# Optimization experiments

Hardware: AMD Instinct MI355X
Metric: run time of the kernel (lower is better)

The kernel has to match this reference:

```python
import jax, jax.numpy as jnp
import numpy as np

B, H, W, C, NUM_HEADS = 32, 8, 128, 512, 8
HK, WK = 7, 11  # local_k
N = H * W
HEAD_DIM = C // NUM_HEADS
SCALE = HEAD_DIM ** (-0.5)


def make_local_mask():
    # key (i,j) is visible to query (h,w) iff i+HK//2 in [h, h+HK) and j+WK//2 in [w, w+WK)
    dh = jnp.arange(H)[None, :] - jnp.arange(H)[:, None] + HK // 2  # [H(query), H(key)]
    dw = jnp.arange(W)[None, :] - jnp.arange(W)[:, None] + WK // 2  # [W(query), W(key)]
    ok_h = (dh >= 0) & (dh < HK)
    ok_w = (dw >= 0) & (dw < WK)
    ok = ok_h[:, None, :, None] & ok_w[None, :, None, :]  # [H,W,H,W]
    return jnp.where(ok.reshape(N, N), 0.0, -jnp.inf).astype(jnp.float32)


def setup_inputs() -> dict:
    key = jax.random.key(0)
    k1, k2, k3 = jax.random.split(key, 3)
    s = C ** (-0.5)
    return {
        "x": jax.random.normal(k1, (B, N, C), dtype=jnp.float32),
        "w_qkv": jax.random.normal(k2, (C, 3 * C), dtype=jnp.float32) * s,
        "w_proj": jax.random.normal(k3, (C, C), dtype=jnp.float32) * s,
        "b_proj": jnp.zeros((C,), dtype=jnp.float32),
    }


def reference(x, w_qkv, w_proj, b_proj):
    mask = make_local_mask()  # [N, N], 0 in window, -inf outside
    b, n, c = x.shape
    qkv = (x @ w_qkv).reshape(b, n, 3, NUM_HEADS, HEAD_DIM)
    qkv = jnp.transpose(qkv, (2, 0, 3, 1, 4))  # [3, B, heads, N, head_dim]
    q, k, v = qkv[0], qkv[1], qkv[2]
    attn = jnp.einsum('bhqd,bhkd->bhqk', q, k) * SCALE + mask
    attn = jax.nn.softmax(attn, axis=-1)
    out = jnp.einsum('bhqk,bhkd->bhqd', attn, v)
    out = jnp.transpose(out, (0, 2, 1, 3)).reshape(b, n, c)
    return out @ w_proj + b_proj
```

## Files before the change

### kernel.cpp

```cpp
#include <hip/hip_runtime.h>

#define Bsz   32
#define Hh    8
#define Ww    128
#define Cc    512
#define NHEAD 8
#define HD    64
#define NN    1024
#define SCALE 0.125f
#define ROWS  1536

typedef _Float16 f16x8 __attribute__((ext_vector_type(8)));
typedef float    f32x4 __attribute__((ext_vector_type(4)));

__device__ __forceinline__ void gload16(const _Float16* g, _Float16* l) {
#if __has_builtin(__builtin_amdgcn_global_load_lds)
  __builtin_amdgcn_global_load_lds(
      (const __attribute__((address_space(1))) unsigned int*)g,
      (__attribute__((address_space(3))) unsigned int*)l, 16, 0, 0);
#else
  *(uint4*)l = *(const uint4*)g;
#endif
}

__global__ __launch_bounds__(256) void tcvt(
    const float* __restrict__ in, _Float16* __restrict__ out, int Nn, int K) {
  const int id = blockIdx.x * 256 + threadIdx.x;
  if (id < Nn * K) {
    const int n = id / K, k = id - n * K;
    out[id] = (_Float16)in[(size_t)k * Nn + n];
  }
}

template<bool A_F32, bool OUT_F16, bool HAS_BIAS>
__global__ __launch_bounds__(256, 2) void gemm_mfma(
    const void* __restrict__ Ap,
    const _Float16* __restrict__ BT,
    const float* __restrict__ bias,
    void* __restrict__ Cout,
    int nbx, int Nn, int K)
{
  __shared__ _Float16 As[2][128 * 32];
  __shared__ _Float16 Bs[2][128 * 32];

  const int wg    = blockIdx.x;
  const int chunk = gridDim.x >> 3;
  const int nid   = (wg & 7) * chunk + (wg >> 3);
  const int bn    = (nid % nbx) * 128;
  const int bm    = (nid / nbx) * 128;

  const int t  = threadIdx.x;
  const int l  = t & 63, wv = t >> 6;
  const int wr = wv >> 1, wc = wv & 1;

  f32x4 acc[4][4] = {};

  const int arow = t >> 2;
  const int ac   = (t & 3) * 8;

  float4 a0, a1, a2, a3;

  const float*    Af = (const float*)Ap;
  const _Float16* Ah = (const _Float16*)Ap;

  auto issueA = [&](int k0) {
    const float* s0 = &Af[(size_t)(bm + arow)      * K + k0 + ac];
    const float* s1 = &Af[(size_t)(bm + arow + 64) * K + k0 + ac];
    a0 = *(const float4*)s0; a1 = *(const float4*)(s0 + 4);
    a2 = *(const float4*)s1; a3 = *(const float4*)(s1 + 4);
  };
  auto writeA = [&](int pb) {
    union { _Float16 h[8]; uint4 u; } p0, p1;
    p0.h[0] = (_Float16)a0.x; p0.h[1] = (_Float16)a0.y;
    p0.h[2] = (_Float16)a0.z; p0.h[3] = (_Float16)a0.w;
    p0.h[4] = (_Float16)a1.x; p0.h[5] = (_Float16)a1.y;
    p0.h[6] = (_Float16)a1.z; p0.h[7] = (_Float16)a1.w;
    p1.h[0] = (_Float16)a2.x; p1.h[1] = (_Float16)a2.y;
    p1.h[2] = (_Float16)a2.z; p1.h[3] = (_Float16)a2.w;
    p1.h[4] = (_Float16)a3.x; p1.h[5] = (_Float16)a3.y;
    p1.h[6] = (_Float16)a3.z; p1.h[7] = (_Float16)a3.w;
    *(uint4*)&As[pb][arow * 32 + ac]        = p0.u;
    *(uint4*)&As[pb][(arow + 64) * 32 + ac] = p1.u;
  };
  auto gloadA = [&](int k0, int pb) {
    gload16(Ah + (size_t)(bm + arow)      * K + k0 + ac, &As[pb][t * 8]);
    gload16(Ah + (size_t)(bm + 64 + arow) * K + k0 + ac, &As[pb][2048 + t * 8]);
  };
  auto gloadB = [&](int k0, int pb) {
    gload16(BT + (size_t)(bn + arow)      * K + k0 + ac, &Bs[pb][t * 8]);
    gload16(BT + (size_t)(bn + 64 + arow) * K + k0 + ac, &Bs[pb][2048 + t * 8]);
  };

  const int nt = K / 32;

  if constexpr (A_F32) { issueA(0); writeA(0); }
  else                 { gloadA(0, 0); }
  gloadB(0, 0);
  __syncthreads();

  int buf = 0;
  for (int tt = 0; tt < nt; ++tt) {
    const int k0n = (tt + 1) * 32;
    const bool more = (tt + 1 < nt);
    if (more) {
      if constexpr (A_F32) issueA(k0n);
      else                 gloadA(k0n, buf ^ 1);
      gloadB(k0n, buf ^ 1);
    }

    const int rA = l & 15, ks = (l >> 4) * 8;
    f16x8 aF[4], bF[4];
#pragma unroll
    for (int i = 0; i < 4; ++i)
      aF[i] = *(const f16x8*)&As[buf][(wr * 64 + i * 16 + rA) * 32 + ks];
#pragma unroll
    for (int j = 0; j < 4; ++j)
      bF[j] = *(const f16x8*)&Bs[buf][(wc * 64 + j * 16 + rA) * 32 + ks];
#pragma unroll
    for (int i = 0; i < 4; ++i)
#pragma unroll
      for (int j = 0; j < 4; ++j)
        acc[i][j] = __builtin_amdgcn_mfma_f32_16x16x32_f16(aF[i], bF[j], acc[i][j], 0, 0, 0);

    if (more) {
      if constexpr (A_F32) writeA(buf ^ 1);
    }
    __syncthreads();
    buf ^= 1;
  }

  const int lc = l & 15, lr4 = (l >> 4) * 4;
#pragma unroll
  for (int i = 0; i < 4; ++i) {
    const size_t row0 = (size_t)(bm + wr * 64 + i * 16 + lr4);
#pragma unroll
    for (int j = 0; j < 4; ++j) {
      const int col = bn + wc * 64 + j * 16 + lc;
      const float bv = HAS_BIAS ? bias[col] : 0.f;
#pragma unroll
      for (int r = 0; r < 4; ++r) {
        const float v = acc[i][j][r] + bv;
        if (OUT_F16)
          ((_Float16*)Cout)[(row0 + r) * Nn + col] = (_Float16)v;
        else
          ((float*)Cout)[(row0 + r) * Nn + col] = v;
      }
    }
  }
}

__global__ __launch_bounds__(512, 4) void local_attn_mfma(
    const _Float16* __restrict__ qkv, _Float16* __restrict__ outh)
{
  const int wg  = blockIdx.x + (Hh / 2) * (blockIdx.y + NHEAD * blockIdx.z);
  const int nid = ((wg & 7) << 7) + (wg >> 3);
  const int hp = nid & 3, head = (nid >> 2) & 7, b = nid >> 5;
  const int h0 = hp * 2;

  const int t = threadIdx.x;
  const int wv = t >> 6, l = t & 63;
  const int g = l >> 4, c = l & 15;
  const int w0 = wv * 16;
  const int kb = min(max(w0 - 8, 0), 96);

  __shared__ _Float16 Vsh[64 * 132];
  __shared__ _Float16 Pbuf[8][576];

  const _Float16* qb = qkv + (size_t)b * NN * ROWS;

  f16x8 qF[2][2];
#pragma unroll
  for (int hi = 0; hi < 2; ++hi) {
    const _Float16* Qg = qb + (size_t)((h0 + hi) * Ww + w0 + c) * ROWS + head * HD;
    qF[hi][0] = *(const f16x8*)&Qg[g * 8];
    qF[hi][1] = *(const f16x8*)&Qg[32 + g * 8];
  }

  float mbias[2][4];
#pragma unroll
  for (int tt = 0; tt < 2; ++tt)
#pragma unroll
    for (int r = 0; r < 4; ++r) {
      const int kcol = kb + 16 * tt + 4 * g + r;
      const int qq   = w0 + c;
      mbias[tt][r] = (kcol >= qq - 5 && kcol <= qq + 5) ? 0.f : -1e30f;
    }

  const int r0 = max(0, h0 - 3), r1 = min(Hh - 1, h0 + 4);
  float m_run[2] = {-1e30f, -1e30f}, s_run[2] = {0.f, 0.f};
  f32x4 accO[2][4] = {};

  const int dd = t & 7, cg = (t & 255) >> 3;

  for (int kr = r0; kr <= r1; ++kr) {
    __syncthreads();
    if (t < 256) {
      f16x8 vr[4];
      const _Float16* Vg = qb + (size_t)(kr * Ww + cg * 4) * ROWS + 2 * Cc + head * HD + dd * 8;
#pragma unroll
      for (int i = 0; i < 4; ++i)
        vr[i] = *(const f16x8*)&Vg[(size_t)i * ROWS];
#pragma unroll
      for (int e = 0; e < 8; ++e) {
        union { _Float16 hh[4]; uint2 u; } pk;
        pk.hh[0] = vr[0][e]; pk.hh[1] = vr[1][e];
        pk.hh[2] = vr[2][e]; pk.hh[3] = vr[3][e];
        *(uint2*)&Vsh[(dd * 8 + e) * 132 + cg * 4] = pk.u;
      }
    }
    __syncthreads();

    const _Float16* Kg = qb + (size_t)(kr * Ww) * ROWS + Cc + head * HD;

#pragma unroll
    for (int hi = 0; hi < 2; ++hi) {
      const int hq = h0 + hi;
      if (kr < hq - 3 || kr > hq + 3) continue;

      f32x4 accS[2] = {};
#pragma unroll
      for (int tt = 0; tt < 2; ++tt) {
        const int col = kb + 16 * tt + c;
#pragma unroll
        for (int s = 0; s < 2; ++s) {
          const f16x8 kF = *(const f16x8*)&Kg[(size_t)col * ROWS + (s * 4 + g) * 8];
          accS[tt] = __builtin_amdgcn_mfma_f32_16x16x32_f16(kF, qF[hi][s], accS[tt], 0, 0, 0);
        }
      }

      float sc[2][4];
      float smax = -1e30f;
#pragma unroll
      for (int tt = 0; tt < 2; ++tt)
#pragma unroll
        for (int r = 0; r < 4; ++r) {
          sc[tt][r] = __builtin_fmaf(accS[tt][r], SCALE, mbias[tt][r]);
          smax = fmaxf(smax, sc[tt][r]);
        }
      smax = fmaxf(smax, __shfl_xor(smax, 16));
      smax = fmaxf(smax, __shfl_xor(smax, 32));
      const float mnew  = fmaxf(m_run[hi], smax);
      const float alpha = __expf(m_run[hi] - mnew);
      m_run[hi] = mnew;

      float ps = 0.f;
#pragma unroll
      for (int tt = 0; tt < 2; ++tt) {
        float p0 = __expf(sc[tt][0] - mnew), p1 = __expf(sc[tt][1] - mnew);
        float p2 = __expf(sc[tt][2] - mnew), p3 = __expf(sc[tt][3] - mnew);
        ps += (p0 + p1) + (p2 + p3);
        union { _Float16 hh[4]; uint2 u; } pk;
        pk.hh[0] = (_Float16)p0; pk.hh[1] = (_Float16)p1;
        pk.hh[2] = (_Float16)p2; pk.hh[3] = (_Float16)p3;
        *(uint2*)&Pbuf[wv][c * 36 + 16 * tt + 4 * g] = pk.u;
      }
      ps += __shfl_xor(ps, 16);
      ps += __shfl_xor(ps, 32);
      s_run[hi] = s_run[hi] * alpha + ps;

      float alr[4];
#pragma unroll
      for (int r = 0; r < 4; ++r)
        alr[r] = __shfl(alpha, 4 * g + r, 16);

      asm volatile("s_waitcnt lgkmcnt(0)" ::: "memory");

      union { f16x8 v; uint2 u2[2]; } pF;
      {
        const _Float16* pp = &Pbuf[wv][c * 36 + g * 8];
        pF.u2[0] = *(const uint2*)pp;
        pF.u2[1] = *(const uint2*)(pp + 4);
      }
#pragma unroll
      for (int jj = 0; jj < 4; ++jj)
#pragma unroll
        for (int r = 0; r < 4; ++r) accO[hi][jj][r] *= alr[r];
#pragma unroll
      for (int jj = 0; jj < 4; ++jj) {
        union { f16x8 v; uint2 u2[2]; } vF;
        const _Float16* vp = &Vsh[(16 * jj + c) * 132 + kb + g * 8];
        vF.u2[0] = *(const uint2*)vp;
        vF.u2[1] = *(const uint2*)(vp + 4);
        accO[hi][jj] = __builtin_amdgcn_mfma_f32_16x16x32_f16(pF.v, vF.v, accO[hi][jj], 0, 0, 0);
      }
    }
  }

#pragma unroll
  for (int hi = 0; hi < 2; ++hi) {
    _Float16* ob = outh + ((size_t)b * NN + (h0 + hi) * Ww + w0) * Cc + head * HD;
#pragma unroll
    for (int r = 0; r < 4; ++r) {
      const float sr  = __shfl(s_run[hi], 4 * g + r, 16);
      const float inv = 1.f / sr;
      const int q = 4 * g + r;
#pragma unroll
      for (int jj = 0; jj < 4; ++jj)
        ob[(size_t)q * Cc + 16 * jj + c] = (_Float16)(accO[hi][jj][r] * inv);
    }
  }
}

extern "C" void kernel_launch(void* const* d_in, const int* in_sizes, int n_in,
                              void* d_out, int out_size, void* d_ws, size_t ws_size,
                              hipStream_t stream)
{
  const float* x      = (const float*)d_in[0];
  const float* w_qkv  = (const float*)d_in[1];
  const float* w_proj = (const float*)d_in[2];
  const float* b_proj = (const float*)d_in[3];
  float* out = (float*)d_out;

  const int M = Bsz * NN;
  char* ws = (char*)d_ws;
  _Float16* qkvh  = (_Float16*)ws;
  _Float16* attnh = (_Float16*)(ws + 100663296);
  _Float16* wqT   = (_Float16*)(ws + 134217728);
  _Float16* wpT   = (_Float16*)(ws + 134217728 + 1572864);

  tcvt<<<(ROWS * Cc + 255) / 256, 256, 0, stream>>>(w_qkv, wqT, ROWS, Cc);
  tcvt<<<(Cc * Cc + 255) / 256, 256, 0, stream>>>(w_proj, wpT, Cc, Cc);

  gemm_mfma<true, true, false><<<(ROWS / 128) * (M / 128), 256, 0, stream>>>(
      x, wqT, nullptr, qkvh, ROWS / 128, ROWS, Cc);

  local_attn_mfma<<<dim3(Hh / 2, NHEAD, Bsz), 512, 0, stream>>>(qkvh, attnh);

  gemm_mfma<false, false, true><<<(Cc / 128) * (M / 128), 256, 0, stream>>>(
      attnh, wpT, b_proj, out, Cc / 128, Cc, Cc);
}
```

Measured before the change: 194.4 us.

## Widen GEMM tiles to 128x256 with 512 threads and prefetch V rows in attention

The two projection GEMMs now use 512-thread blocks covering 128x256 output tiles with eight waves in a 2x4 layout, halving block count and sharing each A tile across more columns. The local attention kernel prefetches the next key row's V into registers while computing the current row, then writes it to shared memory between explicit barriers instead of loading it synchronously at the top of each iteration. It also raises wave priority around the MFMA sections. The risks are higher register pressure from the occupancy-4 launch bound and fewer blocks in flight for the small projection GEMM.

```diff
diff --git a/kernel.cpp b/kernel.cpp
--- a/kernel.cpp
+++ b/kernel.cpp
@@ -33,7 +33,7 @@
 }
 
 template<bool A_F32, bool OUT_F16, bool HAS_BIAS>
-__global__ __launch_bounds__(256, 2) void gemm_mfma(
+__global__ __launch_bounds__(512, 4) void gemm_mfma(
     const void* __restrict__ Ap,
     const _Float16* __restrict__ BT,
     const float* __restrict__ bias,
@@ -41,54 +41,45 @@
     int nbx, int Nn, int K)
 {
   __shared__ _Float16 As[2][128 * 32];
-  __shared__ _Float16 Bs[2][128 * 32];
+  __shared__ _Float16 Bs[2][256 * 32];
 
   const int wg    = blockIdx.x;
   const int chunk = gridDim.x >> 3;
   const int nid   = (wg & 7) * chunk + (wg >> 3);
-  const int bn    = (nid % nbx) * 128;
+  const int bn    = (nid % nbx) * 256;
   const int bm    = (nid / nbx) * 128;
 
   const int t  = threadIdx.x;
   const int l  = t & 63, wv = t >> 6;
-  const int wr = wv >> 1, wc = wv & 1;
+  const int wr = wv >> 2, wc = wv & 3;
 
   f32x4 acc[4][4] = {};
 
   const int arow = t >> 2;
   const int ac   = (t & 3) * 8;
 
-  float4 a0, a1, a2, a3;
-
   const float*    Af = (const float*)Ap;
   const _Float16* Ah = (const _Float16*)Ap;
 
+  float4 a0, a1;
   auto issueA = [&](int k0) {
-    const float* s0 = &Af[(size_t)(bm + arow)      * K + k0 + ac];
-    const float* s1 = &Af[(size_t)(bm + arow + 64) * K + k0 + ac];
+    const float* s0 = &Af[(size_t)(bm + arow) * K + k0 + ac];
     a0 = *(const float4*)s0; a1 = *(const float4*)(s0 + 4);
-    a2 = *(const float4*)s1; a3 = *(const float4*)(s1 + 4);
   };
   auto writeA = [&](int pb) {
-    union { _Float16 h[8]; uint4 u; } p0, p1;
-    p0.h[0] = (_Float16)a0.x; p0.h[1] = (_Float16)a0.y;
-    p0.h[2] = (_Float16)a0.z; p0.h[3] = (_Float16)a0.w;
-    p0.h[4] = (_Float16)a1.x; p0.h[5] = (_Float16)a1.y;
-    p0.h[6] = (_Float16)a1.z; p0.h[7] = (_Float16)a1.w;
-    p1.h[0] = (_Float16)a2.x; p1.h[1] = (_Float16)a2.y;
-    p1.h[2] = (_Float16)a2.z; p1.h[3] = (_Float16)a2.w;
-    p1.h[4] = (_Float16)a3.x; p1.h[5] = (_Float16)a3.y;
-    p1.h[6] = (_Float16)a3.z; p1.h[7] = (_Float16)a3.w;
-    *(uint4*)&As[pb][arow * 32 + ac]        = p0.u;
-    *(uint4*)&As[pb][(arow + 64) * 32 + ac] = p1.u;
+    union { _Float16 h[8]; uint4 u; } pk;
+    pk.h[0] = (_Float16)a0.x; pk.h[1] = (_Float16)a0.y;
+    pk.h[2] = (_Float16)a0.z; pk.h[3] = (_Float16)a0.w;
+    pk.h[4] = (_Float16)a1.x; pk.h[5] = (_Float16)a1.y;
+    pk.h[6] = (_Float16)a1.z; pk.h[7] = (_Float16)a1.w;
+    *(uint4*)&As[pb][arow * 32 + ac] = pk.u;
   };
   auto gloadA = [&](int k0, int pb) {
-    gload16(Ah + (size_t)(bm + arow)      * K + k0 + ac, &As[pb][t * 8]);
-    gload16(Ah + (size_t)(bm + 64 + arow) * K + k0 + ac, &As[pb][2048 + t * 8]);
+    gload16(Ah + (size_t)(bm + arow) * K + k0 + ac, &As[pb][arow * 32 + ac]);
   };
   auto gloadB = [&](int k0, int pb) {
-    gload16(BT + (size_t)(bn + arow)      * K + k0 + ac, &Bs[pb][t * 8]);
-    gload16(BT + (size_t)(bn + 64 + arow) * K + k0 + ac, &Bs[pb][2048 + t * 8]);
+    gload16(BT + (size_t)(bn + arow)       * K + k0 + ac, &Bs[pb][arow * 32 + ac]);
+    gload16(BT + (size_t)(bn + 128 + arow) * K + k0 + ac, &Bs[pb][(128 + arow) * 32 + ac]);
   };
 
   const int nt = K / 32;
@@ -100,12 +91,11 @@
 
   int buf = 0;
   for (int tt = 0; tt < nt; ++tt) {
-    const int k0n = (tt + 1) * 32;
     const bool more = (tt + 1 < nt);
     if (more) {
-      if constexpr (A_F32) issueA(k0n);
-      else                 gloadA(k0n, buf ^ 1);
-      gloadB(k0n, buf ^ 1);
+      if constexpr (A_F32) issueA((tt + 1) * 32);
+      else                 gloadA((tt + 1) * 32, buf ^ 1);
+      gloadB((tt + 1) * 32, buf ^ 1);
     }
 
     const int rA = l & 15, ks = (l >> 4) * 8;
@@ -191,24 +181,31 @@
   f32x4 accO[2][4] = {};
 
   const int dd = t & 7, cg = (t & 255) >> 3;
+  f16x8 vr[4];
+  auto loadV = [&](int kr) {
+    const _Float16* Vg = qb + (size_t)(kr * Ww + cg * 4) * ROWS + 2 * Cc + head * HD + dd * 8;
+#pragma unroll
+    for (int i = 0; i < 4; ++i)
+      vr[i] = *(const f16x8*)&Vg[(size_t)i * ROWS];
+  };
+  auto writeV = [&]() {
+#pragma unroll
+    for (int e = 0; e < 8; ++e) {
+      union { _Float16 hh[4]; uint2 u; } pk;
+      pk.hh[0] = vr[0][e]; pk.hh[1] = vr[1][e];
+      pk.hh[2] = vr[2][e]; pk.hh[3] = vr[3][e];
+      *(uint2*)&Vsh[(dd * 8 + e) * 132 + cg * 4] = pk.u;
+    }
+  };
+
+  if (t < 256) { loadV(r0); writeV(); }
+  asm volatile("s_waitcnt lgkmcnt(0)" ::: "memory");
+  __builtin_amdgcn_s_barrier();
+  __builtin_amdgcn_sched_barrier(0);
 
   for (int kr = r0; kr <= r1; ++kr) {
-    __syncthreads();
-    if (t < 256) {
-      f16x8 vr[4];
-      const _Float16* Vg = qb + (size_t)(kr * Ww + cg * 4) * ROWS + 2 * Cc + head * HD + dd * 8;
-#pragma unroll
-      for (int i = 0; i < 4; ++i)
-        vr[i] = *(const f16x8*)&Vg[(size_t)i * ROWS];
-#pragma unroll
-      for (int e = 0; e < 8; ++e) {
-        union { _Float16 hh[4]; uint2 u; } pk;
-        pk.hh[0] = vr[0][e]; pk.hh[1] = vr[1][e];
-        pk.hh[2] = vr[2][e]; pk.hh[3] = vr[3][e];
-        *(uint2*)&Vsh[(dd * 8 + e) * 132 + cg * 4] = pk.u;
-      }
-    }
-    __syncthreads();
+    const bool more = kr < r1;
+    if (more && t < 256) loadV(kr + 1);
 
     const _Float16* Kg = qb + (size_t)(kr * Ww) * ROWS + Cc + head * HD;
 
@@ -218,6 +215,7 @@
       if (kr < hq - 3 || kr > hq + 3) continue;
 
       f32x4 accS[2] = {};
+      __builtin_amdgcn_s_setprio(1);
 #pragma unroll
       for (int tt = 0; tt < 2; ++tt) {
         const int col = kb + 16 * tt + c;
@@ -227,6 +225,7 @@
           accS[tt] = __builtin_amdgcn_mfma_f32_16x16x32_f16(kF, qF[hi][s], accS[tt], 0, 0, 0);
         }
       }
+      __builtin_amdgcn_s_setprio(0);
 
       float sc[2][4];
       float smax = -1e30f;
@@ -275,6 +274,7 @@
       for (int jj = 0; jj < 4; ++jj)
 #pragma unroll
         for (int r = 0; r < 4; ++r) accO[hi][jj][r] *= alr[r];
+      __builtin_amdgcn_s_setprio(1);
 #pragma unroll
       for (int jj = 0; jj < 4; ++jj) {
         union { f16x8 v; uint2 u2[2]; } vF;
@@ -283,7 +283,15 @@
         vF.u2[1] = *(const uint2*)(vp + 4);
         accO[hi][jj] = __builtin_amdgcn_mfma_f32_16x16x32_f16(pF.v, vF.v, accO[hi][jj], 0, 0, 0);
       }
-    }
+      __builtin_amdgcn_s_setprio(0);
+    }
+
+    __builtin_amdgcn_s_barrier();
+    __builtin_amdgcn_sched_barrier(0);
+    if (more && t < 256) writeV();
+    asm volatile("s_waitcnt lgkmcnt(0)" ::: "memory");
+    __builtin_amdgcn_s_barrier();
+    __builtin_amdgcn_sched_barrier(0);
   }
 
 #pragma unroll
@@ -321,11 +329,11 @@
   tcvt<<<(ROWS * Cc + 255) / 256, 256, 0, stream>>>(w_qkv, wqT, ROWS, Cc);
   tcvt<<<(Cc * Cc + 255) / 256, 256, 0, stream>>>(w_proj, wpT, Cc, Cc);
 
-  gemm_mfma<true, true, false><<<(ROWS / 128) * (M / 128), 256, 0, stream>>>(
-      x, wqT, nullptr, qkvh, ROWS / 128, ROWS, Cc);
+  gemm_mfma<true, true, false><<<(ROWS / 256) * (M / 128), 512, 0, stream>>>(
+      x, wqT, nullptr, qkvh, ROWS / 256, ROWS, Cc);
 
   local_attn_mfma<<<dim3(Hh / 2, NHEAD, Bsz), 512, 0, stream>>>(qkvh, attnh);
 
-  gemm_mfma<false, false, true><<<(Cc / 128) * (M / 128), 256, 0, stream>>>(
-      attnh, wpT, b_proj, out, Cc / 128, Cc, Cc);
-}
+  gemm_mfma<false, false, true><<<(Cc / 256) * (M / 128), 512, 0, stream>>>(
+      attnh, wpT, b_proj, out, Cc / 256, Cc, Cc);
+}
```

Result: no change. 194.6 us (+0.1%).
